# Performance work log

Measured on AMD Instinct MI355X. Metric: run time of the kernel, lower is better.

Reference implementation:

```python
import jax, jax.numpy as jnp
import numpy as np

KERNEL_MUL = 2.0
KERNEL_NUM = 5


def setup_inputs() -> dict:
    key = jax.random.key(0)
    k1, k2 = jax.random.split(key)
    source_features = jax.random.normal(k1, (4096, 1024), dtype=jnp.float32)
    target_features = jax.random.normal(k2, (4096, 1024), dtype=jnp.float32)
    return {"source_features": source_features, "target_features": target_features}


def reference(source_features, target_features):
    n = source_features.shape[0]
    total = jnp.concatenate([source_features, target_features], axis=0)  # [L, D]
    L = total.shape[0]
    # Pairwise squared distances via gram trick (same math as sum((a-b)**2)).
    sq = jnp.sum(total * total, axis=1)  # [L]
    d2 = jnp.maximum(sq[:, None] + sq[None, :] - 2.0 * (total @ total.T), 0.0)  # [L, L]
    # Median-heuristic-style bandwidth: mean of off-diagonal distances.
    bandwidth = jnp.sum(d2) / (L * L - L)
    bandwidth = bandwidth / (KERNEL_MUL ** (KERNEL_NUM // 2))
    # Multi-bandwidth RBF kernel sum (fixed small loop over KERNEL_NUM).
    kernel = jnp.zeros_like(d2)
    for i in range(KERNEL_NUM):
        kernel = kernel + jnp.exp(-d2 / (bandwidth * (KERNEL_MUL ** i)))
    kernel = kernel / KERNEL_NUM
    ss = jnp.mean(kernel[:n, :n])
    tt = jnp.mean(kernel[n:, n:])
    st = jnp.mean(kernel[:n, n:])
    return ss + tt - 2.0 * st
```

## Files before the change

### kernel.cpp

```cpp
#include <hip/hip_runtime.h>
#include <hip/hip_bf16.h>
#include <stdint.h>


#define L_TOTAL 8192
#define D_FEAT  1024
#define N_HALF  4096
#define TILE    128
#define TTILES  64
#define NBLK    (TTILES*(TTILES+1)/2)
#define BK      64

typedef __bf16 bf16_t;
typedef __bf16 bf16x8_t __attribute__((ext_vector_type(8)));
typedef float  f32x4_t  __attribute__((ext_vector_type(4)));

#define XB_OFF   0
#define SQ_OFF   (L_TOTAL * D_FEAT * 2)
#define COL_OFF  (SQ_OFF + L_TOTAL * 4)
#define SACC_OFF (COL_OFF + D_FEAT * 4)
#define C0_OFF   (SACC_OFF + 8)

__device__ __forceinline__ void async_ld16(void* lds, const void* g) {
  auto ldsp = (__attribute__((address_space(3))) void*)(uintptr_t)lds;
  auto gp   = (const __attribute__((address_space(1))) void*)(uintptr_t)g;
  __builtin_amdgcn_global_load_lds(gp, ldsp, 16, 0, 0);
}

extern "C" __global__ __launch_bounds__(256) void k_zero(
    float* __restrict__ colsum, double* __restrict__ S_acc)
{
  const int tid = threadIdx.x;
  for (int c = tid; c < D_FEAT; c += 256) colsum[c] = 0.f;
  if (tid == 0) *S_acc = 0.0;
}

extern "C" __global__ __launch_bounds__(256) void k_prep(
    const float* __restrict__ src, const float* __restrict__ tgt,
    bf16_t* __restrict__ Xb, float* __restrict__ sq, float* __restrict__ colsum)
{
  __shared__ float cs[4][D_FEAT];
  const int tid  = threadIdx.x;
  const int lane = tid & 63;
  const int w    = tid >> 6;
  const int rbase = blockIdx.x * 64 + w * 16;

  float csp[16];
  #pragma unroll
  for (int j = 0; j < 16; ++j) csp[j] = 0.f;

  for (int i = 0; i < 16; ++i) {
    const int row = rbase + i;
    const float* xr = (row < N_HALF) ? (src + (size_t)row * D_FEAT)
                                     : (tgt + (size_t)(row - N_HALF) * D_FEAT);
    const float4* xv = (const float4*)(xr + lane * 16);
    float4 v[4];
    #pragma unroll
    for (int q = 0; q < 4; ++q) v[q] = xv[q];

    bf16x8_t b0, b1;
    float s = 0.f;
    #pragma unroll
    for (int q = 0; q < 4; ++q) {
      const float f0 = v[q].x, f1 = v[q].y, f2 = v[q].z, f3 = v[q].w;
      bf16_t c0 = (bf16_t)f0, c1 = (bf16_t)f1, c2 = (bf16_t)f2, c3 = (bf16_t)f3;
      if (q < 2) { b0[q*4+0]=c0; b0[q*4+1]=c1; b0[q*4+2]=c2; b0[q*4+3]=c3; }
      else       { b1[(q-2)*4+0]=c0; b1[(q-2)*4+1]=c1; b1[(q-2)*4+2]=c2; b1[(q-2)*4+3]=c3; }
      float g0=(float)c0, g1=(float)c1, g2=(float)c2, g3=(float)c3;
      s += g0*g0 + g1*g1 + g2*g2 + g3*g3;
      csp[q*4+0] += f0; csp[q*4+1] += f1; csp[q*4+2] += f2; csp[q*4+3] += f3;
    }
    bf16_t* xb = Xb + (size_t)row * D_FEAT + lane * 16;
    *(bf16x8_t*)xb = b0;
    *(bf16x8_t*)(xb + 8) = b1;

    #pragma unroll
    for (int off = 32; off > 0; off >>= 1) s += __shfl_down(s, off);
    if (lane == 0) sq[row] = s;
  }

  #pragma unroll
  for (int j = 0; j < 16; ++j) cs[w][lane * 16 + j] = csp[j];
  __syncthreads();
  #pragma unroll
  for (int k = 0; k < 4; ++k) {
    const int c = tid * 4 + k;
    atomicAdd(&colsum[c], cs[0][c] + cs[1][c] + cs[2][c] + cs[3][c]);
  }
}

extern "C" __global__ __launch_bounds__(1024) void k_bw(
    const float* __restrict__ sq, const float* __restrict__ colsum,
    float* __restrict__ c0out)
{
  const int tid = threadIdx.x;
  double t = 0.0;
  for (int i = tid; i < L_TOTAL; i += 1024) t += (double)sq[i];
  t *= 2.0 * (double)L_TOTAL;
  if (tid < D_FEAT) { double v = colsum[tid]; t -= 2.0 * v * v; }
  __shared__ double red[1024];
  red[tid] = t;
  __syncthreads();
  for (int off = 512; off > 0; off >>= 1) {
    if (tid < off) red[tid] += red[tid + off];
    __syncthreads();
  }
  if (tid == 0) {
    double bw = red[0] / ((double)L_TOTAL * (double)L_TOTAL - (double)L_TOTAL);
    bw = bw / 4.0;
    *c0out = (float)(1.4426950408889634 / bw);
  }
}

extern "C" __global__ __launch_bounds__(256) void k_mmd(
    const bf16_t* __restrict__ Xb, const float* __restrict__ sq,
    const float* __restrict__ c0ptr, double* __restrict__ S_acc)
{
  __shared__ bf16_t As[TILE * BK];
  __shared__ bf16_t Bs[TILE * BK];
  __shared__ float  red[256];

  const int b = (blockIdx.x & 7) * (NBLK / 8) + (blockIdx.x >> 3);
  int ti = (int)((sqrtf(8.f * (float)b + 1.f) - 1.f) * 0.5f);
  while ((ti + 1) * (ti + 2) / 2 <= b) ++ti;
  while (ti * (ti + 1) / 2 > b) --ti;
  const int tj = b - ti * (ti + 1) / 2;
  const int row0 = ti * TILE, col0 = tj * TILE;

  const int tid  = threadIdx.x;
  const int lane = tid & 63;
  const int w    = tid >> 6;
  const int wr   = w >> 1, wc = w & 1;

  f32x4_t acc[4][4] = {};

  const int srow = lane >> 3;
  const int scol = ((lane & 7) ^ srow) * 8;

  for (int k0 = 0; k0 < D_FEAT; k0 += BK) {
    #pragma unroll
    for (int q = 0; q < 4; ++q) {
      const int ch = w * 4 + q;
      const bf16_t* gA = Xb + (size_t)(row0 + ch * 8 + srow) * D_FEAT + k0 + scol;
      const bf16_t* gB = Xb + (size_t)(col0 + ch * 8 + srow) * D_FEAT + k0 + scol;
      async_ld16(&As[ch * 512], gA);
      async_ld16(&Bs[ch * 512], gB);
    }
    __syncthreads();

    bf16x8_t af[2][4], bfr[2][4];
    #pragma unroll
    for (int kk = 0; kk < 2; ++kk) {
      const int slot = kk * 4 + (lane >> 4);
      #pragma unroll
      for (int m = 0; m < 4; ++m) {
        const int r = wr * 64 + m * 16 + (lane & 15);
        af[kk][m] = *(const bf16x8_t*)&As[r * BK + (slot ^ (r & 7)) * 8];
      }
      #pragma unroll
      for (int n = 0; n < 4; ++n) {
        const int r = wc * 64 + n * 16 + (lane & 15);
        bfr[kk][n] = *(const bf16x8_t*)&Bs[r * BK + (slot ^ (r & 7)) * 8];
      }
    }
    #pragma unroll
    for (int kk = 0; kk < 2; ++kk)
      #pragma unroll
      for (int m = 0; m < 4; ++m)
        #pragma unroll
        for (int n = 0; n < 4; ++n)
          acc[m][n] = __builtin_amdgcn_mfma_f32_16x16x32_bf16(af[kk][m], bfr[kk][n], acc[m][n], 0, 0, 0);
    __syncthreads();
  }

  const float c0   = *c0ptr;
  const float sgn  = ((ti < TTILES / 2) == (tj < TTILES / 2)) ? 1.f : -1.f;
  const float wgt  = (ti == tj ? 1.f : 2.f) * sgn;
  float part = 0.f;
  const int colb = col0 + wc * 64 + (lane & 15);
  const int rowb = row0 + wr * 64 + (lane >> 4) * 4;
  #pragma unroll
  for (int m = 0; m < 4; ++m) {
    #pragma unroll
    for (int n = 0; n < 4; ++n) {
      const float sqj = sq[colb + n * 16];
      #pragma unroll
      for (int r = 0; r < 4; ++r) {
        const float sqi = sq[rowb + m * 16 + r];
        float d2 = sqi + sqj - 2.f * acc[m][n][r];
        d2 = fmaxf(d2, 0.f);
        const float t  = d2 * c0;
        const float e  = __builtin_amdgcn_exp2f(-0.0625f * t);
        const float e2 = e * e, e4 = e2 * e2, e8 = e4 * e4, e16 = e8 * e8;
        part += e + e2 + e4 + e8 + e16;
      }
    }
  }
  part *= wgt;

  red[tid] = part;
  __syncthreads();
  for (int off = 128; off > 0; off >>= 1) {
    if (tid < off) red[tid] += red[tid + off];
    __syncthreads();
  }
  if (tid == 0) atomicAdd(S_acc, (double)red[0]);
}

extern "C" __global__ void k_fin(const double* __restrict__ S_acc, float* __restrict__ out)
{
  out[0] = (float)(*S_acc / (5.0 * (double)N_HALF * (double)N_HALF));
}

extern "C" void kernel_launch(void* const* d_in, const int* in_sizes, int n_in,
                              void* d_out, int out_size, void* d_ws, size_t ws_size,
                              hipStream_t stream) {
  const float* src = (const float*)d_in[0];
  const float* tgt = (const float*)d_in[1];
  float* out = (float*)d_out;
  char* ws = (char*)d_ws;
  bf16_t* Xb     = (bf16_t*)(ws + XB_OFF);
  float*  sq     = (float*)(ws + SQ_OFF);
  float*  colsum = (float*)(ws + COL_OFF);
  double* S_acc  = (double*)(ws + SACC_OFF);
  float*  c0     = (float*)(ws + C0_OFF);

  k_zero<<<1, 256, 0, stream>>>(colsum, S_acc);
  k_prep<<<128, 256, 0, stream>>>(src, tgt, Xb, sq, colsum);
  k_bw  <<<1, 1024, 0, stream>>>(sq, colsum, c0);
  k_mmd <<<NBLK, 256, 0, stream>>>(Xb, sq, c0, S_acc);
  k_fin <<<1, 1, 0, stream>>>(S_acc, out);
}
```

Measured before the change: 214.8 us.

## Coalesce prep loads, double prep grid, precompute LDS addresses, shuffle-reduce in MMD

The prep kernel now reads each row with lane-strided float4 loads, which coalesce across the wave, and writes bf16x4 vectors. Its grid doubles to 256 blocks of 32 rows each. The MMD kernel precomputes the global and LDS fragment addresses outside the k-loop and folds the exp scale into a single constant. It also replaces the block-wide LDS tree reduction with a wave shuffle reduction plus a 4-entry LDS sum. Together these target address arithmetic, prep-kernel memory efficiency and epilogue synchronisation, while the GEMM structure stays the same.

```diff
diff --git a/kernel.cpp b/kernel.cpp
--- a/kernel.cpp
+++ b/kernel.cpp
@@ -12,6 +12,7 @@
 #define BK      64
 
 typedef __bf16 bf16_t;
+typedef __bf16 bf16x4_t __attribute__((ext_vector_type(4)));
 typedef __bf16 bf16x8_t __attribute__((ext_vector_type(8)));
 typedef float  f32x4_t  __attribute__((ext_vector_type(4)));
 
@@ -19,7 +20,7 @@
 #define SQ_OFF   (L_TOTAL * D_FEAT * 2)
 #define COL_OFF  (SQ_OFF + L_TOTAL * 4)
 #define SACC_OFF (COL_OFF + D_FEAT * 4)
-#define C0_OFF   (SACC_OFF + 8)
+#define C1_OFF   (SACC_OFF + 8)
 
 __device__ __forceinline__ void async_ld16(void* lds, const void* g) {
   auto ldsp = (__attribute__((address_space(3))) void*)(uintptr_t)lds;
@@ -43,44 +44,38 @@
   const int tid  = threadIdx.x;
   const int lane = tid & 63;
   const int w    = tid >> 6;
-  const int rbase = blockIdx.x * 64 + w * 16;
+  const int rbase = blockIdx.x * 32 + w * 8;
 
   float csp[16];
   #pragma unroll
   for (int j = 0; j < 16; ++j) csp[j] = 0.f;
 
-  for (int i = 0; i < 16; ++i) {
+  for (int i = 0; i < 8; ++i) {
     const int row = rbase + i;
     const float* xr = (row < N_HALF) ? (src + (size_t)row * D_FEAT)
                                      : (tgt + (size_t)(row - N_HALF) * D_FEAT);
-    const float4* xv = (const float4*)(xr + lane * 16);
-    float4 v[4];
-    #pragma unroll
-    for (int q = 0; q < 4; ++q) v[q] = xv[q];
-
-    bf16x8_t b0, b1;
     float s = 0.f;
     #pragma unroll
     for (int q = 0; q < 4; ++q) {
-      const float f0 = v[q].x, f1 = v[q].y, f2 = v[q].z, f3 = v[q].w;
-      bf16_t c0 = (bf16_t)f0, c1 = (bf16_t)f1, c2 = (bf16_t)f2, c3 = (bf16_t)f3;
-      if (q < 2) { b0[q*4+0]=c0; b0[q*4+1]=c1; b0[q*4+2]=c2; b0[q*4+3]=c3; }
-      else       { b1[(q-2)*4+0]=c0; b1[(q-2)*4+1]=c1; b1[(q-2)*4+2]=c2; b1[(q-2)*4+3]=c3; }
-      float g0=(float)c0, g1=(float)c1, g2=(float)c2, g3=(float)c3;
-      s += g0*g0 + g1*g1 + g2*g2 + g3*g3;
-      csp[q*4+0] += f0; csp[q*4+1] += f1; csp[q*4+2] += f2; csp[q*4+3] += f3;
-    }
-    bf16_t* xb = Xb + (size_t)row * D_FEAT + lane * 16;
-    *(bf16x8_t*)xb = b0;
-    *(bf16x8_t*)(xb + 8) = b1;
-
+      const float4 v = ((const float4*)xr)[q * 64 + lane];
+      bf16x4_t bv;
+      bv[0] = (bf16_t)v.x; bv[1] = (bf16_t)v.y; bv[2] = (bf16_t)v.z; bv[3] = (bf16_t)v.w;
+      *(bf16x4_t*)(Xb + (size_t)row * D_FEAT + (q * 64 + lane) * 4) = bv;
+      const float g0 = (float)bv[0], g1 = (float)bv[1], g2 = (float)bv[2], g3 = (float)bv[3];
+      s += g0 * g0 + g1 * g1 + g2 * g2 + g3 * g3;
+      csp[q * 4 + 0] += v.x; csp[q * 4 + 1] += v.y;
+      csp[q * 4 + 2] += v.z; csp[q * 4 + 3] += v.w;
+    }
     #pragma unroll
     for (int off = 32; off > 0; off >>= 1) s += __shfl_down(s, off);
     if (lane == 0) sq[row] = s;
   }
 
   #pragma unroll
-  for (int j = 0; j < 16; ++j) cs[w][lane * 16 + j] = csp[j];
+  for (int q = 0; q < 4; ++q) {
+    float4 v4 = make_float4(csp[q*4+0], csp[q*4+1], csp[q*4+2], csp[q*4+3]);
+    *(float4*)&cs[w][(q * 64 + lane) * 4] = v4;
+  }
   __syncthreads();
   #pragma unroll
   for (int k = 0; k < 4; ++k) {
@@ -91,7 +86,7 @@
 
 extern "C" __global__ __launch_bounds__(1024) void k_bw(
     const float* __restrict__ sq, const float* __restrict__ colsum,
-    float* __restrict__ c0out)
+    float* __restrict__ c1out)
 {
   const int tid = threadIdx.x;
   double t = 0.0;
@@ -108,17 +103,17 @@
   if (tid == 0) {
     double bw = red[0] / ((double)L_TOTAL * (double)L_TOTAL - (double)L_TOTAL);
     bw = bw / 4.0;
-    *c0out = (float)(1.4426950408889634 / bw);
+    *c1out = (float)(-1.4426950408889634 / (16.0 * bw));
   }
 }
 
 extern "C" __global__ __launch_bounds__(256) void k_mmd(
     const bf16_t* __restrict__ Xb, const float* __restrict__ sq,
-    const float* __restrict__ c0ptr, double* __restrict__ S_acc)
-{
-  __shared__ bf16_t As[TILE * BK];
-  __shared__ bf16_t Bs[TILE * BK];
-  __shared__ float  red[256];
+    const float* __restrict__ c1ptr, double* __restrict__ S_acc)
+{
+  __shared__ __align__(16) char smem[2 * TILE * BK * 2];
+  bf16_t* As = (bf16_t*)smem;
+  bf16_t* Bs = (bf16_t*)(smem + TILE * BK * 2);
 
   const int b = (blockIdx.x & 7) * (NBLK / 8) + (blockIdx.x >> 3);
   int ti = (int)((sqrtf(8.f * (float)b + 1.f) - 1.f) * 0.5f);
@@ -132,53 +127,64 @@
   const int w    = tid >> 6;
   const int wr   = w >> 1, wc = w & 1;
 
-  f32x4_t acc[4][4] = {};
-
   const int srow = lane >> 3;
   const int scol = ((lane & 7) ^ srow) * 8;
+  uint32_t offA[4], offB[4];
+  #pragma unroll
+  for (int q = 0; q < 4; ++q) {
+    const int ch = w * 4 + q;
+    offA[q] = (uint32_t)(row0 + ch * 8 + srow) * D_FEAT + scol;
+    offB[q] = (uint32_t)(col0 + ch * 8 + srow) * D_FEAT + scol;
+  }
+
+  const int x = lane >> 4, y = lane & 7, rlo = lane & 15;
+  const int baA0 = (wr * 64 + rlo) * (BK * 2) + ((x ^ y) * 16);
+  const int baB0 = (wc * 64 + rlo) * (BK * 2) + ((x ^ y) * 16);
+  const int baA1 = baA0 ^ 64;
+  const int baB1 = baB0 ^ 64;
+  const char* Ac = (const char*)As;
+  const char* Bc = (const char*)Bs;
+
+  f32x4_t acc[4][4] = {};
 
   for (int k0 = 0; k0 < D_FEAT; k0 += BK) {
     #pragma unroll
     for (int q = 0; q < 4; ++q) {
-      const int ch = w * 4 + q;
-      const bf16_t* gA = Xb + (size_t)(row0 + ch * 8 + srow) * D_FEAT + k0 + scol;
-      const bf16_t* gB = Xb + (size_t)(col0 + ch * 8 + srow) * D_FEAT + k0 + scol;
-      async_ld16(&As[ch * 512], gA);
-      async_ld16(&Bs[ch * 512], gB);
+      async_ld16(&As[(w * 4 + q) * 512], Xb + offA[q] + k0);
+      async_ld16(&Bs[(w * 4 + q) * 512], Xb + offB[q] + k0);
     }
     __syncthreads();
 
-    bf16x8_t af[2][4], bfr[2][4];
-    #pragma unroll
-    for (int kk = 0; kk < 2; ++kk) {
-      const int slot = kk * 4 + (lane >> 4);
+    bf16x8_t af0[4], af1[4], bf0[4], bf1[4];
+    #pragma unroll
+    for (int m = 0; m < 4; ++m) {
+      af0[m] = *(const bf16x8_t*)(Ac + baA0 + m * 2048);
+      af1[m] = *(const bf16x8_t*)(Ac + baA1 + m * 2048);
+    }
+    #pragma unroll
+    for (int n = 0; n < 4; ++n) {
+      bf0[n] = *(const bf16x8_t*)(Bc + baB0 + n * 2048);
+      bf1[n] = *(const bf16x8_t*)(Bc + baB1 + n * 2048);
+    }
+    #pragma unroll
+    for (int m = 0; m < 4; ++m)
       #pragma unroll
-      for (int m = 0; m < 4; ++m) {
-        const int r = wr * 64 + m * 16 + (lane & 15);
-        af[kk][m] = *(const bf16x8_t*)&As[r * BK + (slot ^ (r & 7)) * 8];
-      }
+      for (int n = 0; n < 4; ++n)
+        acc[m][n] = __builtin_amdgcn_mfma_f32_16x16x32_bf16(af0[m], bf0[n], acc[m][n], 0, 0, 0);
+    #pragma unroll
+    for (int m = 0; m < 4; ++m)
       #pragma unroll
-      for (int n = 0; n < 4; ++n) {
-        const int r = wc * 64 + n * 16 + (lane & 15);
-        bfr[kk][n] = *(const bf16x8_t*)&Bs[r * BK + (slot ^ (r & 7)) * 8];
-      }
-    }
-    #pragma unroll
-    for (int kk = 0; kk < 2; ++kk)
-      #pragma unroll
-      for (int m = 0; m < 4; ++m)
-        #pragma unroll
-        for (int n = 0; n < 4; ++n)
-          acc[m][n] = __builtin_amdgcn_mfma_f32_16x16x32_bf16(af[kk][m], bfr[kk][n], acc[m][n], 0, 0, 0);
+      for (int n = 0; n < 4; ++n)
+        acc[m][n] = __builtin_amdgcn_mfma_f32_16x16x32_bf16(af1[m], bf1[n], acc[m][n], 0, 0, 0);
     __syncthreads();
   }
 
-  const float c0   = *c0ptr;
+  const float c1   = *c1ptr;
   const float sgn  = ((ti < TTILES / 2) == (tj < TTILES / 2)) ? 1.f : -1.f;
   const float wgt  = (ti == tj ? 1.f : 2.f) * sgn;
   float part = 0.f;
-  const int colb = col0 + wc * 64 + (lane & 15);
-  const int rowb = row0 + wr * 64 + (lane >> 4) * 4;
+  const int colb = col0 + wc * 64 + rlo;
+  const int rowb = row0 + wr * 64 + x * 4;
   #pragma unroll
   for (int m = 0; m < 4; ++m) {
     #pragma unroll
@@ -187,10 +193,8 @@
       #pragma unroll
       for (int r = 0; r < 4; ++r) {
         const float sqi = sq[rowb + m * 16 + r];
-        float d2 = sqi + sqj - 2.f * acc[m][n][r];
-        d2 = fmaxf(d2, 0.f);
-        const float t  = d2 * c0;
-        const float e  = __builtin_amdgcn_exp2f(-0.0625f * t);
+        float d2 = fmaxf(sqi + sqj - 2.f * acc[m][n][r], 0.f);
+        const float e  = __builtin_amdgcn_exp2f(d2 * c1);
         const float e2 = e * e, e4 = e2 * e2, e8 = e4 * e4, e16 = e8 * e8;
         part += e + e2 + e4 + e8 + e16;
       }
@@ -198,13 +202,14 @@
   }
   part *= wgt;
 
-  red[tid] = part;
-  __syncthreads();
-  for (int off = 128; off > 0; off >>= 1) {
-    if (tid < off) red[tid] += red[tid + off];
-    __syncthreads();
-  }
-  if (tid == 0) atomicAdd(S_acc, (double)red[0]);
+  #pragma unroll
+  for (int off = 32; off > 0; off >>= 1) part += __shfl_down(part, off);
+  float* red = (float*)smem;
+  __syncthreads();
+  if (lane == 0) red[w] = part;
+  __syncthreads();
+  if (tid == 0)
+    atomicAdd(S_acc, (double)(red[0] + red[1] + red[2] + red[3]));
 }
 
 extern "C" __global__ void k_fin(const double* __restrict__ S_acc, float* __restrict__ out)
@@ -223,11 +228,11 @@
   float*  sq     = (float*)(ws + SQ_OFF);
   float*  colsum = (float*)(ws + COL_OFF);
   double* S_acc  = (double*)(ws + SACC_OFF);
-  float*  c0     = (float*)(ws + C0_OFF);
+  float*  c1     = (float*)(ws + C1_OFF);
 
   k_zero<<<1, 256, 0, stream>>>(colsum, S_acc);
-  k_prep<<<128, 256, 0, stream>>>(src, tgt, Xb, sq, colsum);
-  k_bw  <<<1, 1024, 0, stream>>>(sq, colsum, c0);
-  k_mmd <<<NBLK, 256, 0, stream>>>(Xb, sq, c0, S_acc);
+  k_prep<<<256, 256, 0, stream>>>(src, tgt, Xb, sq, colsum);
+  k_bw  <<<1, 1024, 0, stream>>>(sq, colsum, c1);
+  k_mmd <<<NBLK, 256, 0, stream>>>(Xb, sq, c1, S_acc);
   k_fin <<<1, 1, 0, stream>>>(S_acc, out);
 }
```

Measured after the change: 221.6 us. +3.2%, slower.
